# Kernel tuning notes

Hardware: AMD Instinct MI355X
Metric: run time of the kernel (lower is better)

Reference implementation:

```python
import jax, jax.numpy as jnp
import numpy as np

LN_EPS = 1e-5

def layer_norm(h, gamma, beta):
    mu = jnp.mean(h, axis=-1, keepdims=True)
    var = jnp.mean(jnp.square(h - mu), axis=-1, keepdims=True)
    return (h - mu) * jax.lax.rsqrt(var + LN_EPS) * gamma + beta

def gcn_conv(x, src, dst, W, b, n_nodes):
    # PyG GCNConv: h = X W; out = D^-1/2 (A + I) D^-1/2 h + b
    h = x @ W
    deg = jax.ops.segment_sum(jnp.ones_like(src, dtype=h.dtype), dst, num_segments=n_nodes)
    dinv = jax.lax.rsqrt(jnp.maximum(deg, 1.0))  # deg >= 1 due to self-loops
    norm = dinv[src] * dinv[dst]                  # [E]
    msg = h[src] * norm[:, None]                  # [E, d]
    return jax.ops.segment_sum(msg, dst, num_segments=n_nodes) + b

def setup_inputs() -> dict:
    key = jax.random.key(0)
    ks = jax.random.split(key, 8)
    N, E, Cin, Ch, Cout = 10000, 160000, 256, 512, 256
    x = jax.random.normal(ks[0], (N, Cin), dtype=jnp.float32)
    edge_index = jax.random.randint(ks[1], (2, E), 0, N, dtype=jnp.int64)
    W1 = jax.random.normal(ks[2], (Cin, Ch), dtype=jnp.float32) * (1.0 / np.sqrt(Cin))
    b1 = jnp.zeros((Ch,), dtype=jnp.float32)
    gamma1 = jnp.ones((Ch,), dtype=jnp.float32)
    beta1 = jnp.zeros((Ch,), dtype=jnp.float32)
    W2 = jax.random.normal(ks[3], (Ch, Cout), dtype=jnp.float32) * (1.0 / np.sqrt(Ch))
    b2 = jnp.zeros((Cout,), dtype=jnp.float32)
    gamma2 = jnp.ones((Cout,), dtype=jnp.float32)
    beta2 = jnp.zeros((Cout,), dtype=jnp.float32)
    return {"x": x, "edge_index": edge_index, "W1": W1, "b1": b1,
            "gamma1": gamma1, "beta1": beta1, "W2": W2, "b2": b2,
            "gamma2": gamma2, "beta2": beta2}

def reference(x, edge_index, W1, b1, gamma1, beta1, W2, b2, gamma2, beta2):
    n = x.shape[0]
    loops = jnp.arange(n, dtype=edge_index.dtype)
    src = jnp.concatenate([edge_index[0], loops])
    dst = jnp.concatenate([edge_index[1], loops])
    h = gcn_conv(x, src, dst, W1, b1, n)
    h = jax.nn.relu(layer_norm(h, gamma1, beta1))  # dropout = identity (eval mode)
    g = gcn_conv(h, src, dst, W2, b2, n)
    g = jax.nn.relu(layer_norm(g, gamma2, beta2))
    return g
```

## Files before the change

kernel.cpp:

```cpp
#include <hip/hip_runtime.h>
#include <hip/hip_bf16.h>


typedef __attribute__((ext_vector_type(8))) short bf16x8;
typedef __attribute__((ext_vector_type(4))) float f32x4;
typedef __attribute__((ext_vector_type(4))) unsigned short us4;
typedef __attribute__((ext_vector_type(8))) unsigned short us8;

__device__ __forceinline__ unsigned short f2bf(float f) {
  unsigned int x = __float_as_uint(f);
  return (unsigned short)((x + 0x7FFFu + ((x >> 16) & 1u)) >> 16);
}
__device__ __forceinline__ float bf2f(unsigned short u) {
  return __uint_as_float((unsigned int)u << 16);
}


__device__ __forceinline__ void transpose_tile(const float* __restrict__ W,
                                               unsigned short* __restrict__ Wt,
                                               int K, int N, int n0, int k0,
                                               unsigned short (*t)[33], int tid) {
  int tx = tid & 31, ty = tid >> 5;
#pragma unroll
  for (int i = 0; i < 32; i += 8)
    t[ty + i][tx] = f2bf(W[(size_t)(k0 + ty + i) * N + n0 + tx]);
  __syncthreads();
#pragma unroll
  for (int i = 0; i < 32; i += 8)
    Wt[(size_t)(n0 + ty + i) * K + k0 + tx] = t[tx][ty + i];
}

__global__ __launch_bounds__(256) void prep_kernel(
    const float* __restrict__ x, unsigned short* __restrict__ xb, long nelem,
    const int* __restrict__ dst, int E, int* __restrict__ deg,
    const float* __restrict__ W1, unsigned short* __restrict__ W1t,
    const float* __restrict__ W2, unsigned short* __restrict__ W2t,
    int Cin, int Ch, int Cout, int nbx, int nbe, int nbw1) {
  __shared__ unsigned short t[32][33];
  int bid = blockIdx.x;
  int tid = threadIdx.x;
  if (bid < nbx) {
    long i = ((long)bid * 256 + tid) * 8;
    if (i + 8 <= nelem) {
      f32x4 a = *(const f32x4*)&x[i];
      f32x4 b = *(const f32x4*)&x[i + 4];
      us8 o;
      o[0] = f2bf(a.x); o[1] = f2bf(a.y); o[2] = f2bf(a.z); o[3] = f2bf(a.w);
      o[4] = f2bf(b.x); o[5] = f2bf(b.y); o[6] = f2bf(b.z); o[7] = f2bf(b.w);
      *(us8*)&xb[i] = o;
    }
  } else if (bid < nbx + nbe) {
    int e = (bid - nbx) * 256 + tid;
    if (e < E) atomicAdd(&deg[dst[e]], 1);
  } else if (bid < nbx + nbe + nbw1) {
    int ti = bid - nbx - nbe;
    int w1w = Ch >> 5;
    transpose_tile(W1, W1t, Cin, Ch, (ti % w1w) * 32, (ti / w1w) * 32, t, tid);
  } else {
    int ti = bid - nbx - nbe - nbw1;
    int w2w = Cout >> 5;
    transpose_tile(W2, W2t, Ch, Cout, (ti % w2w) * 32, (ti / w2w) * 32, t, tid);
  }
}

__global__ __launch_bounds__(1024) void scan_kernel(const int* __restrict__ deg, int N,
                                                    int* __restrict__ offsets,
                                                    int* __restrict__ curs,
                                                    float* __restrict__ dinv) {
  __shared__ int wsum[16];
  __shared__ int chunk_base;
  int tid = threadIdx.x;
  int lane = tid & 63, wid = tid >> 6;
  if (tid == 0) chunk_base = 0;
  __syncthreads();
  for (int c = 0; c < N; c += 1024) {
    int i = c + tid;
    int v = (i < N) ? deg[i] : 0;
    if (i < N) dinv[i] = rsqrtf((float)(v + 1));
    int s = v;
#pragma unroll
    for (int off = 1; off < 64; off <<= 1) {
      int t = __shfl_up(s, off, 64);
      if (lane >= off) s += t;
    }
    if (lane == 63) wsum[wid] = s;
    __syncthreads();
    if (wid == 0 && lane < 16) {
      int ws = wsum[lane];
      int t = ws;
#pragma unroll
      for (int off = 1; off < 16; off <<= 1) {
        int u = __shfl_up(t, off, 64);
        if (lane >= off) t += u;
      }
      wsum[lane] = t - ws;
    }
    __syncthreads();
    if (i < N) {
      int o = chunk_base + wsum[wid] + s - v;
      offsets[i] = o;
      curs[i] = o;
    }
    __syncthreads();
    if (tid == 1023) chunk_base += wsum[15] + s;
  }
  __syncthreads();
  if (tid == 0) offsets[N] = chunk_base;
}

__global__ __launch_bounds__(256) void fill_kernel(const int* __restrict__ src,
                                                   const int* __restrict__ dst, int E,
                                                   int* __restrict__ curs,
                                                   const float* __restrict__ dinv,
                                                   int* __restrict__ csr_src,
                                                   float* __restrict__ csr_norm) {
  int e = blockIdx.x * 256 + threadIdx.x;
  if (e >= E) return;
  int s = src[e], d = dst[e];
  int p = atomicAdd(&curs[d], 1);
  csr_src[p]  = s;
  csr_norm[p] = dinv[s] * dinv[d];
}


template <bool FUSE_LN, typename OutT>
__global__ __launch_bounds__(256) void agg_kernel(const unsigned short* __restrict__ H,
                                                  const int* __restrict__ csr_src,
                                                  const float* __restrict__ csr_norm,
                                                  const int* __restrict__ offsets,
                                                  const float* __restrict__ dinv,
                                                  const float* __restrict__ bias,
                                                  const float* __restrict__ gamma,
                                                  const float* __restrict__ beta,
                                                  OutT* __restrict__ out) {
  __shared__ f32x4 sh[256];
  int node = blockIdx.x;
  int tid = threadIdx.x, w = tid >> 6, c4 = tid & 63;
  int p0 = offsets[node], p1 = offsets[node + 1];
  f32x4 acc = {0.f, 0.f, 0.f, 0.f};
  for (int p = p0 + w; p < p1; p += 4) {
    int s    = csr_src[p];
    float wt = csr_norm[p];
    us4 hv = *(const us4*)&H[(size_t)s * 256 + c4 * 4];
    acc.x = fmaf(bf2f(hv.x), wt, acc.x);
    acc.y = fmaf(bf2f(hv.y), wt, acc.y);
    acc.z = fmaf(bf2f(hv.z), wt, acc.z);
    acc.w = fmaf(bf2f(hv.w), wt, acc.w);
  }
  sh[tid] = acc;
  __syncthreads();
  if (tid < 64) {
    f32x4 a = sh[tid] + sh[64 + tid] + sh[128 + tid] + sh[192 + tid];
    float dn = dinv[node];
    float w2 = dn * dn;
    us4 sv = *(const us4*)&H[(size_t)node * 256 + tid * 4];
    a.x = fmaf(bf2f(sv.x), w2, a.x);
    a.y = fmaf(bf2f(sv.y), w2, a.y);
    a.z = fmaf(bf2f(sv.z), w2, a.z);
    a.w = fmaf(bf2f(sv.w), w2, a.w);
    if (bias) a += *(const f32x4*)&bias[tid * 4];
    if constexpr (FUSE_LN) {
      float s  = a.x + a.y + a.z + a.w;
      float ss = a.x * a.x + a.y * a.y + a.z * a.z + a.w * a.w;
#pragma unroll
      for (int off = 32; off > 0; off >>= 1) {
        s  += __shfl_xor(s, off, 64);
        ss += __shfl_xor(ss, off, 64);
      }
      float mu = s * (1.0f / 256.0f);
      float var = ss * (1.0f / 256.0f) - mu * mu;
      float r = rsqrtf(var + 1e-5f);
      f32x4 g  = *(const f32x4*)&gamma[tid * 4];
      f32x4 be = *(const f32x4*)&beta[tid * 4];
      f32x4 o;
      o.x = fmaxf((a.x - mu) * r * g.x + be.x, 0.f);
      o.y = fmaxf((a.y - mu) * r * g.y + be.y, 0.f);
      o.z = fmaxf((a.z - mu) * r * g.z + be.z, 0.f);
      o.w = fmaxf((a.w - mu) * r * g.w + be.w, 0.f);
      *(f32x4*)&out[(size_t)node * 256 + tid * 4] = o;
    } else {
      us4 o;
      o.x = f2bf(a.x); o.y = f2bf(a.y); o.z = f2bf(a.z); o.w = f2bf(a.w);
      *(us4*)&out[(size_t)node * 256 + tid * 4] = o;
    }
  }
}


template <typename OutT>
__global__ __launch_bounds__(256) void mfma_gemm_kernel(
    const unsigned short* __restrict__ A, const unsigned short* __restrict__ Bt,
    const float* __restrict__ bias, OutT* __restrict__ C, int M, int K, int N) {
  __shared__ unsigned short As[128 * 32];
  __shared__ unsigned short Bs[128 * 32];
  int tid = threadIdx.x;
  int lane = tid & 63, wid = tid >> 6;
  int bm = blockIdx.x * 128, bn = blockIdx.y * 128;
  int wm = (wid >> 1) * 64, wn = (wid & 1) * 64;
  int srow = tid >> 2;
  int schunk = tid & 3;
  int frow = lane & 15, fk = lane >> 4;
  f32x4 acc[4][4] = {};

  for (int k0 = 0; k0 < K; k0 += 32) {
#pragma unroll
    for (int r = 0; r < 2; ++r) {
      int row = r * 64 + srow;
      int scA = schunk ^ ((row >> 1) & 3);
      int ga = bm + row; ga = ga < M ? ga : M - 1;
      int gb = bn + row; gb = gb < N ? gb : N - 1;
      const unsigned short* gA = A + (size_t)ga * K + k0 + scA * 8;
      const unsigned short* gB = Bt + (size_t)gb * K + k0 + scA * 8;
      __builtin_amdgcn_global_load_lds(
          (const __attribute__((address_space(1))) unsigned int*)(const void*)gA,
          (__attribute__((address_space(3))) unsigned int*)(void*)(As + (r * 64 + wid * 16) * 32),
          16, 0, 0);
      __builtin_amdgcn_global_load_lds(
          (const __attribute__((address_space(1))) unsigned int*)(const void*)gB,
          (__attribute__((address_space(3))) unsigned int*)(void*)(Bs + (r * 64 + wid * 16) * 32),
          16, 0, 0);
    }
    __syncthreads();
    bf16x8 af[4], bf[4];
#pragma unroll
    for (int mi = 0; mi < 4; ++mi) {
      int row = wm + mi * 16 + frow;
      int sc = fk ^ ((row >> 1) & 3);
      af[mi] = *(const bf16x8*)(As + row * 32 + sc * 8);
    }
#pragma unroll
    for (int ni = 0; ni < 4; ++ni) {
      int row = wn + ni * 16 + frow;
      int sc = fk ^ ((row >> 1) & 3);
      bf[ni] = *(const bf16x8*)(Bs + row * 32 + sc * 8);
    }
#pragma unroll
    for (int mi = 0; mi < 4; ++mi)
#pragma unroll
      for (int ni = 0; ni < 4; ++ni)
        acc[mi][ni] = __builtin_amdgcn_mfma_f32_16x16x32_bf16(af[mi], bf[ni], acc[mi][ni], 0, 0, 0);
    __syncthreads();
  }

  int row0 = bm + wm + (lane >> 4) * 4;
  int col0 = bn + wn + (lane & 15);
#pragma unroll
  for (int mi = 0; mi < 4; ++mi) {
#pragma unroll
    for (int ni = 0; ni < 4; ++ni) {
      int col = col0 + ni * 16;
      float bv = bias ? bias[col] : 0.0f;
#pragma unroll
      for (int r = 0; r < 4; ++r) {
        int row = row0 + mi * 16 + r;
        if (row < M) {
          float v = acc[mi][ni][r] + bv;
          if constexpr (sizeof(OutT) == 4) C[(size_t)row * N + col] = v;
          else                             C[(size_t)row * N + col] = f2bf(v);
        }
      }
    }
  }
}


__global__ __launch_bounds__(256) void ln_relu512_kernel(const float* __restrict__ in,
                                                         const float* __restrict__ gamma,
                                                         const float* __restrict__ beta,
                                                         unsigned short* __restrict__ out) {
  int row = blockIdx.x;
  const float* p = in + (size_t)row * 512;
  int tid = threadIdx.x;
  float v0 = p[tid];
  float v1 = p[tid + 256];
  float s = v0 + v1;
  float ss = v0 * v0 + v1 * v1;
#pragma unroll
  for (int off = 32; off > 0; off >>= 1) {
    s  += __shfl_down(s, off, 64);
    ss += __shfl_down(ss, off, 64);
  }
  __shared__ float sh[8];
  int wid = tid >> 6;
  if ((tid & 63) == 0) { sh[wid] = s; sh[4 + wid] = ss; }
  __syncthreads();
  s  = sh[0] + sh[1] + sh[2] + sh[3];
  ss = sh[4] + sh[5] + sh[6] + sh[7];
  float mu = s * (1.0f / 512.0f);
  float var = ss * (1.0f / 512.0f) - mu * mu;
  float r = rsqrtf(var + 1e-5f);
  out[(size_t)row * 512 + tid]       = f2bf(fmaxf((v0 - mu) * r * gamma[tid] + beta[tid], 0.0f));
  out[(size_t)row * 512 + tid + 256] = f2bf(fmaxf((v1 - mu) * r * gamma[tid + 256] + beta[tid + 256], 0.0f));
}


extern "C" void kernel_launch(void* const* d_in, const int* in_sizes, int n_in,
                              void* d_out, int out_size, void* d_ws, size_t ws_size,
                              hipStream_t stream) {
  const float* x    = (const float*)d_in[0];
  const int*   ei   = (const int*)d_in[1];
  const float* W1   = (const float*)d_in[2];
  const float* b1   = (const float*)d_in[3];
  const float* ga1  = (const float*)d_in[4];
  const float* be1  = (const float*)d_in[5];
  const float* W2   = (const float*)d_in[6];
  const float* b2   = (const float*)d_in[7];
  const float* ga2  = (const float*)d_in[8];
  const float* be2  = (const float*)d_in[9];
  float* out = (float*)d_out;

  const int Ch   = in_sizes[3];
  const int Cout = in_sizes[7];
  const int Cin  = in_sizes[2] / Ch;
  const int N    = in_sizes[0] / Cin;
  const int E    = in_sizes[1] / 2;
  const int* srcp = ei;
  const int* dstp = ei + E;

  char* ws = (char*)d_ws;
  size_t off = 0;
  auto alloc = [&](size_t bytes) -> void* {
    off = (off + 255) & ~(size_t)255;
    void* p = ws + off;
    off += bytes;
    return p;
  };
  unsigned short* xb   = (unsigned short*)alloc((size_t)N * Cin * 2);
  unsigned short* axb  = (unsigned short*)alloc((size_t)N * Cin * 2);
  float*          h1   = (float*)alloc((size_t)N * Ch * 4);
  unsigned short* h1b  = (unsigned short*)alloc((size_t)N * Ch * 2);
  unsigned short* h2b  = (unsigned short*)alloc((size_t)N * Cout * 2);
  unsigned short* W1t  = (unsigned short*)alloc((size_t)Cin * Ch * 2);
  unsigned short* W2t  = (unsigned short*)alloc((size_t)Ch * Cout * 2);
  int*   deg   = (int*)alloc((size_t)N * 4);
  int*   curs  = (int*)alloc((size_t)N * 4);
  int*   offs  = (int*)alloc((size_t)(N + 1) * 4);
  float* dinv  = (float*)alloc((size_t)N * 4);
  int*   csr_s = (int*)alloc((size_t)E * 4);
  float* csr_n = (float*)alloc((size_t)E * 4);

  hipMemsetAsync(deg, 0, (size_t)N * 4, stream);

  long nelem = (long)N * Cin;
  int nbx  = (int)((nelem / 8 + 255) / 256);
  int nbe  = (E + 255) / 256;
  int nbw1 = (Cin / 32) * (Ch / 32);
  int nbw2 = (Ch / 32) * (Cout / 32);
  prep_kernel<<<nbx + nbe + nbw1 + nbw2, 256, 0, stream>>>(
      x, xb, nelem, dstp, E, deg, W1, W1t, W2, W2t, Cin, Ch, Cout, nbx, nbe, nbw1);
  scan_kernel<<<1, 1024, 0, stream>>>(deg, N, offs, curs, dinv);
  fill_kernel<<<nbe, 256, 0, stream>>>(srcp, dstp, E, curs, dinv, csr_s, csr_n);

  agg_kernel<false, unsigned short><<<N, 256, 0, stream>>>(
      xb, csr_s, csr_n, offs, dinv, nullptr, nullptr, nullptr, axb);
  mfma_gemm_kernel<float><<<dim3((N + 127) / 128, Ch / 128), 256, 0, stream>>>(
      axb, W1t, b1, h1, N, Cin, Ch);
  ln_relu512_kernel<<<N, 256, 0, stream>>>(h1, ga1, be1, h1b);

  mfma_gemm_kernel<unsigned short><<<dim3((N + 127) / 128, Cout / 128), 256, 0, stream>>>(
      h1b, W2t, nullptr, h2b, N, Ch, Cout);
  agg_kernel<true, float><<<N, 256, 0, stream>>>(
      h2b, csr_s, csr_n, offs, dinv, b2, ga2, be2, out);
}
```

Measured before the change: 208.4 us.

## Map one wave per node in aggregation and shrink GEMM M-tile to 64

```diff
diff --git a/kernel.cpp b/kernel.cpp
--- a/kernel.cpp
+++ b/kernel.cpp
@@ -14,7 +14,6 @@
 __device__ __forceinline__ float bf2f(unsigned short u) {
   return __uint_as_float((unsigned int)u << 16);
 }
-
 
 __device__ __forceinline__ void transpose_tile(const float* __restrict__ W,
                                                unsigned short* __restrict__ Wt,
@@ -132,57 +131,52 @@
                                                   const float* __restrict__ bias,
                                                   const float* __restrict__ gamma,
                                                   const float* __restrict__ beta,
-                                                  OutT* __restrict__ out) {
-  __shared__ f32x4 sh[256];
-  int node = blockIdx.x;
-  int tid = threadIdx.x, w = tid >> 6, c4 = tid & 63;
+                                                  OutT* __restrict__ out, int N) {
+  int node = blockIdx.x * 4 + (threadIdx.x >> 6);
+  if (node >= N) return;
+  int lane = threadIdx.x & 63;
   int p0 = offsets[node], p1 = offsets[node + 1];
   f32x4 acc = {0.f, 0.f, 0.f, 0.f};
-  for (int p = p0 + w; p < p1; p += 4) {
+  for (int p = p0; p < p1; ++p) {
     int s    = csr_src[p];
     float wt = csr_norm[p];
-    us4 hv = *(const us4*)&H[(size_t)s * 256 + c4 * 4];
+    us4 hv = *(const us4*)&H[(size_t)s * 256 + lane * 4];
     acc.x = fmaf(bf2f(hv.x), wt, acc.x);
     acc.y = fmaf(bf2f(hv.y), wt, acc.y);
     acc.z = fmaf(bf2f(hv.z), wt, acc.z);
     acc.w = fmaf(bf2f(hv.w), wt, acc.w);
   }
-  sh[tid] = acc;
-  __syncthreads();
-  if (tid < 64) {
-    f32x4 a = sh[tid] + sh[64 + tid] + sh[128 + tid] + sh[192 + tid];
-    float dn = dinv[node];
-    float w2 = dn * dn;
-    us4 sv = *(const us4*)&H[(size_t)node * 256 + tid * 4];
-    a.x = fmaf(bf2f(sv.x), w2, a.x);
-    a.y = fmaf(bf2f(sv.y), w2, a.y);
-    a.z = fmaf(bf2f(sv.z), w2, a.z);
-    a.w = fmaf(bf2f(sv.w), w2, a.w);
-    if (bias) a += *(const f32x4*)&bias[tid * 4];
-    if constexpr (FUSE_LN) {
-      float s  = a.x + a.y + a.z + a.w;
-      float ss = a.x * a.x + a.y * a.y + a.z * a.z + a.w * a.w;
-#pragma unroll
-      for (int off = 32; off > 0; off >>= 1) {
-        s  += __shfl_xor(s, off, 64);
-        ss += __shfl_xor(ss, off, 64);
-      }
-      float mu = s * (1.0f / 256.0f);
-      float var = ss * (1.0f / 256.0f) - mu * mu;
-      float r = rsqrtf(var + 1e-5f);
-      f32x4 g  = *(const f32x4*)&gamma[tid * 4];
-      f32x4 be = *(const f32x4*)&beta[tid * 4];
-      f32x4 o;
-      o.x = fmaxf((a.x - mu) * r * g.x + be.x, 0.f);
-      o.y = fmaxf((a.y - mu) * r * g.y + be.y, 0.f);
-      o.z = fmaxf((a.z - mu) * r * g.z + be.z, 0.f);
-      o.w = fmaxf((a.w - mu) * r * g.w + be.w, 0.f);
-      *(f32x4*)&out[(size_t)node * 256 + tid * 4] = o;
-    } else {
-      us4 o;
-      o.x = f2bf(a.x); o.y = f2bf(a.y); o.z = f2bf(a.z); o.w = f2bf(a.w);
-      *(us4*)&out[(size_t)node * 256 + tid * 4] = o;
-    }
+  float dn = dinv[node];
+  float w2 = dn * dn;
+  us4 sv = *(const us4*)&H[(size_t)node * 256 + lane * 4];
+  acc.x = fmaf(bf2f(sv.x), w2, acc.x);
+  acc.y = fmaf(bf2f(sv.y), w2, acc.y);
+  acc.z = fmaf(bf2f(sv.z), w2, acc.z);
+  acc.w = fmaf(bf2f(sv.w), w2, acc.w);
+  if (bias) acc += *(const f32x4*)&bias[lane * 4];
+  if constexpr (FUSE_LN) {
+    float s  = acc.x + acc.y + acc.z + acc.w;
+    float ss = acc.x * acc.x + acc.y * acc.y + acc.z * acc.z + acc.w * acc.w;
+#pragma unroll
+    for (int off = 32; off > 0; off >>= 1) {
+      s  += __shfl_xor(s, off, 64);
+      ss += __shfl_xor(ss, off, 64);
+    }
+    float mu = s * (1.0f / 256.0f);
+    float var = ss * (1.0f / 256.0f) - mu * mu;
+    float r = rsqrtf(var + 1e-5f);
+    f32x4 g  = *(const f32x4*)&gamma[lane * 4];
+    f32x4 be = *(const f32x4*)&beta[lane * 4];
+    f32x4 o;
+    o.x = fmaxf((acc.x - mu) * r * g.x + be.x, 0.f);
+    o.y = fmaxf((acc.y - mu) * r * g.y + be.y, 0.f);
+    o.z = fmaxf((acc.z - mu) * r * g.z + be.z, 0.f);
+    o.w = fmaxf((acc.w - mu) * r * g.w + be.w, 0.f);
+    *(f32x4*)&out[(size_t)node * 256 + lane * 4] = o;
+  } else {
+    us4 o;
+    o.x = f2bf(acc.x); o.y = f2bf(acc.y); o.z = f2bf(acc.z); o.w = f2bf(acc.w);
+    *(us4*)&out[(size_t)node * 256 + lane * 4] = o;
   }
 }
 
@@ -191,39 +185,42 @@
 __global__ __launch_bounds__(256) void mfma_gemm_kernel(
     const unsigned short* __restrict__ A, const unsigned short* __restrict__ Bt,
     const float* __restrict__ bias, OutT* __restrict__ C, int M, int K, int N) {
-  __shared__ unsigned short As[128 * 32];
+  __shared__ unsigned short As[64 * 32];
   __shared__ unsigned short Bs[128 * 32];
   int tid = threadIdx.x;
   int lane = tid & 63, wid = tid >> 6;
-  int bm = blockIdx.x * 128, bn = blockIdx.y * 128;
-  int wm = (wid >> 1) * 64, wn = (wid & 1) * 64;
+  int bm = blockIdx.x * 64, bn = blockIdx.y * 128;
+  int wm = (wid >> 1) * 32, wn = (wid & 1) * 64;
   int srow = tid >> 2;
   int schunk = tid & 3;
   int frow = lane & 15, fk = lane >> 4;
-  f32x4 acc[4][4] = {};
+  f32x4 acc[2][4] = {};
 
   for (int k0 = 0; k0 < K; k0 += 32) {
+    {
+      int row = srow;
+      int scA = schunk ^ ((row >> 1) & 3);
+      int ga = bm + row; ga = ga < M ? ga : M - 1;
+      const unsigned short* gA = A + (size_t)ga * K + k0 + scA * 8;
+      __builtin_amdgcn_global_load_lds(
+          (const __attribute__((address_space(1))) unsigned int*)(const void*)gA,
+          (__attribute__((address_space(3))) unsigned int*)(void*)(As + (wid * 16) * 32),
+          16, 0, 0);
+    }
 #pragma unroll
     for (int r = 0; r < 2; ++r) {
       int row = r * 64 + srow;
-      int scA = schunk ^ ((row >> 1) & 3);
-      int ga = bm + row; ga = ga < M ? ga : M - 1;
-      int gb = bn + row; gb = gb < N ? gb : N - 1;
-      const unsigned short* gA = A + (size_t)ga * K + k0 + scA * 8;
-      const unsigned short* gB = Bt + (size_t)gb * K + k0 + scA * 8;
-      __builtin_amdgcn_global_load_lds(
-          (const __attribute__((address_space(1))) unsigned int*)(const void*)gA,
-          (__attribute__((address_space(3))) unsigned int*)(void*)(As + (r * 64 + wid * 16) * 32),
-          16, 0, 0);
+      int scB = schunk ^ ((row >> 1) & 3);
+      const unsigned short* gB = Bt + (size_t)(bn + row) * K + k0 + scB * 8;
       __builtin_amdgcn_global_load_lds(
           (const __attribute__((address_space(1))) unsigned int*)(const void*)gB,
           (__attribute__((address_space(3))) unsigned int*)(void*)(Bs + (r * 64 + wid * 16) * 32),
           16, 0, 0);
     }
     __syncthreads();
-    bf16x8 af[4], bf[4];
-#pragma unroll
-    for (int mi = 0; mi < 4; ++mi) {
+    bf16x8 af[2], bf[4];
+#pragma unroll
+    for (int mi = 0; mi < 2; ++mi) {
       int row = wm + mi * 16 + frow;
       int sc = fk ^ ((row >> 1) & 3);
       af[mi] = *(const bf16x8*)(As + row * 32 + sc * 8);
@@ -235,17 +232,17 @@
       bf[ni] = *(const bf16x8*)(Bs + row * 32 + sc * 8);
     }
 #pragma unroll
-    for (int mi = 0; mi < 4; ++mi)
+    for (int mi = 0; mi < 2; ++mi)
 #pragma unroll
       for (int ni = 0; ni < 4; ++ni)
         acc[mi][ni] = __builtin_amdgcn_mfma_f32_16x16x32_bf16(af[mi], bf[ni], acc[mi][ni], 0, 0, 0);
     __syncthreads();
   }
 
-  int row0 = bm + wm + (lane >> 4) * 4;
-  int col0 = bn + wn + (lane & 15);
-#pragma unroll
-  for (int mi = 0; mi < 4; ++mi) {
+  int row0 = bm + wm + fk * 4;
+  int col0 = bn + wn + frow;
+#pragma unroll
+  for (int mi = 0; mi < 2; ++mi) {
 #pragma unroll
     for (int ni = 0; ni < 4; ++ni) {
       int col = col0 + ni * 16;
@@ -351,14 +348,14 @@
   scan_kernel<<<1, 1024, 0, stream>>>(deg, N, offs, curs, dinv);
   fill_kernel<<<nbe, 256, 0, stream>>>(srcp, dstp, E, curs, dinv, csr_s, csr_n);
 
-  agg_kernel<false, unsigned short><<<N, 256, 0, stream>>>(
-      xb, csr_s, csr_n, offs, dinv, nullptr, nullptr, nullptr, axb);
-  mfma_gemm_kernel<float><<<dim3((N + 127) / 128, Ch / 128), 256, 0, stream>>>(
+  agg_kernel<false, unsigned short><<<(N + 3) / 4, 256, 0, stream>>>(
+      xb, csr_s, csr_n, offs, dinv, nullptr, nullptr, nullptr, axb, N);
+  mfma_gemm_kernel<float><<<dim3((N + 63) / 64, Ch / 128), 256, 0, stream>>>(
       axb, W1t, b1, h1, N, Cin, Ch);
   ln_relu512_kernel<<<N, 256, 0, stream>>>(h1, ga1, be1, h1b);
 
-  mfma_gemm_kernel<unsigned short><<<dim3((N + 127) / 128, Cout / 128), 256, 0, stream>>>(
+  mfma_gemm_kernel<unsigned short><<<dim3((N + 63) / 64, Cout / 128), 256, 0, stream>>>(
       h1b, W2t, nullptr, h2b, N, Ch, Cout);
-  agg_kernel<true, float><<<N, 256, 0, stream>>>(
-      h2b, csr_s, csr_n, offs, dinv, b2, ga2, be2, out);
-}
+  agg_kernel<true, float><<<(N + 3) / 4, 256, 0, stream>>>(
+      h2b, csr_s, csr_n, offs, dinv, b2, ga2, be2, out, N);
+}
```

Measured after the change: 204.9 us. About the same (-1.7%).
